# Performance work log

Measured on AMD Instinct MI355X. Metric: run time of the kernel, lower is better.

Reference implementation:

```python
import jax, jax.numpy as jnp
import numpy as np

B, T, C = 4, 2048, 1024
H, D = 16, 64  # num_heads, head_dim; H*D == C

def setup_inputs() -> dict:
    key = jax.random.key(0)
    ks = jax.random.split(key, 5)
    s = 0.02
    return {
        "x": jax.random.normal(ks[0], (B, T, C), dtype=jnp.float32),
        "W_qkv": jax.random.normal(ks[1], (C, 3 * C), dtype=jnp.float32) * s,
        "b_qkv": jnp.zeros((3 * C,), dtype=jnp.float32),
        "W_out": jax.random.normal(ks[2], (C, C), dtype=jnp.float32) * s,
        "b_out": jnp.zeros((C,), dtype=jnp.float32),
    }

def reference(x, W_qkv, b_qkv, W_out, b_out):
    Bx, Tx, Cx = x.shape
    qkv = x @ W_qkv + b_qkv                       # [B,T,3C]
    q, k, v = jnp.split(qkv, 3, axis=-1)
    def heads(t):
        return t.reshape(Bx, Tx, H, D).transpose(0, 2, 1, 3)  # [B,H,T,D]
    q, k, v = heads(q), heads(k), heads(v)
    scale = 1.0 / jnp.sqrt(jnp.float32(D))
    attn = jnp.einsum('bhqd,bhkd->bhqk', q, k) * scale
    causal = jnp.tril(jnp.ones((Tx, Tx), dtype=bool))  # True = keep
    attn = jnp.where(causal, attn, -jnp.inf)
    attn = jax.nn.softmax(attn, axis=-1)
    out = jnp.einsum('bhqk,bhkd->bhqd', attn, v)  # [B,H,T,D]
    out = out.transpose(0, 2, 1, 3).reshape(Bx, Tx, Cx)
    return out @ W_out + b_out
```

## Files before the change

### kernel.cpp

```cpp
#include <hip/hip_runtime.h>
#include <math.h>

typedef unsigned short u16;
using bf16x8   = __attribute__((ext_vector_type(8))) __bf16;
using floatx4  = __attribute__((ext_vector_type(4))) float;
using ushortx8 = __attribute__((ext_vector_type(8))) unsigned short;
using ushortx4 = __attribute__((ext_vector_type(4))) unsigned short;
using uintx4   = __attribute__((ext_vector_type(4))) unsigned int;
using uintx2   = __attribute__((ext_vector_type(2))) unsigned int;

static __device__ __forceinline__ u16 f2bf(float f) {
  return (u16)((__float_as_uint(f) + 0x8000u) >> 16);
}
static __device__ __forceinline__ unsigned int pk2bf(float lo, float hi) {
#if __has_builtin(__builtin_amdgcn_cvt_pk_bf16_f32)
  typedef __attribute__((ext_vector_type(2))) __bf16 bf16x2_t;
  bf16x2_t r = __builtin_amdgcn_cvt_pk_bf16_f32(lo, hi);
  return *(unsigned int*)&r;
#else
  return __builtin_amdgcn_perm(__float_as_uint(hi) + 0x8000u,
                               __float_as_uint(lo) + 0x8000u, 0x07060302u);
#endif
}
static __device__ __forceinline__ float fast_exp2(float x) {
#if __has_builtin(__builtin_amdgcn_exp2f)
  return __builtin_amdgcn_exp2f(x);
#else
  return exp2f(x);
#endif
}
static __device__ __forceinline__ float fast_rcp(float x) {
#if __has_builtin(__builtin_amdgcn_rcpf)
  return __builtin_amdgcn_rcpf(x);
#else
  return 1.0f / x;
#endif
}
static __device__ __forceinline__ void gload_lds16(const void* g, void* l) {
  __builtin_amdgcn_global_load_lds(
      (const __attribute__((address_space(1))) unsigned int*)g,
      (__attribute__((address_space(3))) unsigned int*)l, 16, 0, 0);
}

static __device__ __forceinline__ void transW_tile(
    const float* __restrict__ W, u16* __restrict__ WT, int K, int N,
    int bx, int by, float (*tile)[68], int t) {
  const int kb = by * 64, nb = bx * 64;
  {
    const int kl = t >> 2, nc = (t & 3) * 16;
    const float* src = W + (size_t)(kb + kl) * N + nb + nc;
    #pragma unroll
    for (int c = 0; c < 4; c++)
      *(floatx4*)&tile[kl][nc + c * 4] = *(const floatx4*)(src + c * 4);
  }
  __syncthreads();
  {
    const int nl = t >> 2, kc = (t & 3) * 16;
    uintx4 u0, u1;
    #pragma unroll
    for (int j = 0; j < 4; j++)
      u0[j] = pk2bf(tile[kc + 2 * j][nl], tile[kc + 2 * j + 1][nl]);
    #pragma unroll
    for (int j = 0; j < 4; j++)
      u1[j] = pk2bf(tile[kc + 8 + 2 * j][nl], tile[kc + 9 + 2 * j][nl]);
    u16* dst = WT + (size_t)(nb + nl) * K + kb + kc;
    *(uintx4*)dst = u0;
    *(uintx4*)(dst + 8) = u1;
  }
}

__global__ __launch_bounds__(256) void prep(
    const float* __restrict__ x, const float* __restrict__ Wqkv,
    const float* __restrict__ Wout, u16* __restrict__ Xb,
    u16* __restrict__ WqT, u16* __restrict__ WoT) {
  __shared__ float tile[64][68];
  const int blk = blockIdx.x;
  const int t = threadIdx.x;
  if (blk < 4096) {
    const int i = (blk * 256 + t) * 8;
    floatx4 f0 = *(const floatx4*)(x + i);
    floatx4 f1 = *(const floatx4*)(x + i + 4);
    uintx4 u;
    u[0] = pk2bf(f0[0], f0[1]); u[1] = pk2bf(f0[2], f0[3]);
    u[2] = pk2bf(f1[0], f1[1]); u[3] = pk2bf(f1[2], f1[3]);
    *(uintx4*)(Xb + i) = u;
  } else if (blk < 4096 + 768) {
    const int b2 = blk - 4096;
    transW_tile(Wqkv, WqT, 1024, 3072, b2 % 48, b2 / 48, tile, t);
  } else {
    const int b3 = blk - 4096 - 768;
    transW_tile(Wout, WoT, 1024, 1024, b3 % 16, b3 / 16, tile, t);
  }
}

template <int OUT>
__global__ __launch_bounds__(256) void gemm128(
    const u16* __restrict__ A, const u16* __restrict__ Bt,
    const float* __restrict__ bias,
    u16* __restrict__ Qb, u16* __restrict__ Kb, u16* __restrict__ Vt,
    float* __restrict__ Out, int N, int K)
{
  __shared__ u16 As[128 * 64];
  __shared__ u16 Bs[128 * 64];

  const int tid  = threadIdx.x;
  const int wave = tid >> 6, lane = tid & 63;
  const int quad = lane >> 4, l15 = lane & 15;
  const int lrow = lane >> 3;
  const int scol = ((lane & 7) ^ lrow) * 8;

  const int rowBase = blockIdx.y * 128;
  const int colBase = blockIdx.x * 128;
  const int wRow = (wave >> 1) * 64;
  const int wCol = (wave & 1) * 64;

  floatx4 acc[4][4];
  #pragma unroll
  for (int i = 0; i < 4; i++)
    #pragma unroll
    for (int j = 0; j < 4; j++)
      acc[i][j] = floatx4{0.f, 0.f, 0.f, 0.f};

  const u16* Ap = A  + (size_t)(rowBase + (wave * 4) * 8 + lrow) * K + scol;
  const u16* Bp = Bt + (size_t)(colBase + (wave * 4) * 8 + lrow) * K + scol;

  const bool swapped = (OUT == 1) || (colBase < 2048);

  if (swapped) {
    for (int k0 = 0; k0 < K; k0 += 64) {
      __syncthreads();
      #pragma unroll
      for (int i = 0; i < 4; i++) {
        const int c = wave * 4 + i;
        gload_lds16(Ap + (size_t)(i * 8) * K + k0, &As[c * 512]);
        gload_lds16(Bp + (size_t)(i * 8) * K + k0, &Bs[c * 512]);
      }
      __syncthreads();
      #pragma unroll
      for (int ks = 0; ks < 2; ks++) {
        const int sw = (((ks << 2) | quad) ^ (l15 & 7)) << 3;
        bf16x8 a[4], b[4];
        #pragma unroll
        for (int mt = 0; mt < 4; mt++)
          a[mt] = *(const bf16x8*)&As[(wRow + mt * 16 + l15) * 64 + sw];
        #pragma unroll
        for (int nt = 0; nt < 4; nt++)
          b[nt] = *(const bf16x8*)&Bs[(wCol + nt * 16 + l15) * 64 + sw];
        #pragma unroll
        for (int nt = 0; nt < 4; nt++)
          #pragma unroll
          for (int mt = 0; mt < 4; mt++)
            acc[nt][mt] = __builtin_amdgcn_mfma_f32_16x16x32_bf16(b[nt], a[mt], acc[nt][mt], 0, 0, 0);
      }
    }
    if constexpr (OUT == 0) {
      const int which = colBase >> 10;
      const float qscale = 0.18033688011112042f;
      #pragma unroll
      for (int nt = 0; nt < 4; nt++) {
        const int gn0 = colBase + wCol + nt * 16 + quad * 4;
        const floatx4 bv = *(const floatx4*)&bias[gn0];
        const int gl0 = (gn0 & 1023);
        const int h = gl0 >> 6, d0 = gl0 & 63;
        #pragma unroll
        for (int mt = 0; mt < 4; mt++) {
          const int gm = rowBase + wRow + mt * 16 + l15;
          const int bb = gm >> 11, t0 = gm & 2047;
          const int bh = bb * 16 + h;
          uintx2 w;
          if (which == 0) {
            w[0] = pk2bf((acc[nt][mt][0] + bv[0]) * qscale, (acc[nt][mt][1] + bv[1]) * qscale);
            w[1] = pk2bf((acc[nt][mt][2] + bv[2]) * qscale, (acc[nt][mt][3] + bv[3]) * qscale);
            *(uintx2*)&Qb[((size_t)bh * 2048 + t0) * 64 + d0] = w;
          } else {
            w[0] = pk2bf(acc[nt][mt][0] + bv[0], acc[nt][mt][1] + bv[1]);
            w[1] = pk2bf(acc[nt][mt][2] + bv[2], acc[nt][mt][3] + bv[3]);
            *(uintx2*)&Kb[((size_t)bh * 2048 + t0) * 64 + d0] = w;
          }
        }
      }
    } else {
      #pragma unroll
      for (int nt = 0; nt < 4; nt++) {
        const int gn0 = colBase + wCol + nt * 16 + quad * 4;
        const floatx4 bv = *(const floatx4*)&bias[gn0];
        #pragma unroll
        for (int mt = 0; mt < 4; mt++) {
          const int gm = rowBase + wRow + mt * 16 + l15;
          floatx4 v = acc[nt][mt] + bv;
          *(floatx4*)&Out[(size_t)gm * N + gn0] = v;
        }
      }
    }
  } else {
    for (int k0 = 0; k0 < K; k0 += 64) {
      __syncthreads();
      #pragma unroll
      for (int i = 0; i < 4; i++) {
        const int c = wave * 4 + i;
        gload_lds16(Ap + (size_t)(i * 8) * K + k0, &As[c * 512]);
        gload_lds16(Bp + (size_t)(i * 8) * K + k0, &Bs[c * 512]);
      }
      __syncthreads();
      #pragma unroll
      for (int ks = 0; ks < 2; ks++) {
        const int sw = (((ks << 2) | quad) ^ (l15 & 7)) << 3;
        bf16x8 a[4], b[4];
        #pragma unroll
        for (int mt = 0; mt < 4; mt++)
          a[mt] = *(const bf16x8*)&As[(wRow + mt * 16 + l15) * 64 + sw];
        #pragma unroll
        for (int nt = 0; nt < 4; nt++)
          b[nt] = *(const bf16x8*)&Bs[(wCol + nt * 16 + l15) * 64 + sw];
        #pragma unroll
        for (int mt = 0; mt < 4; mt++)
          #pragma unroll
          for (int nt = 0; nt < 4; nt++)
            acc[mt][nt] = __builtin_amdgcn_mfma_f32_16x16x32_bf16(a[mt], b[nt], acc[mt][nt], 0, 0, 0);
      }
    }
    #pragma unroll
    for (int mt = 0; mt < 4; mt++) {
      const int gm0 = rowBase + wRow + mt * 16 + quad * 4;
      const int bb = gm0 >> 11, t0 = gm0 & 2047;
      #pragma unroll
      for (int nt = 0; nt < 4; nt++) {
        const int gn = colBase + wCol + nt * 16 + l15;
        const int gl = gn & 1023;
        const float bv = bias[gn];
        const int h = gl >> 6, d = gl & 63;
        const int bh = bb * 16 + h;
        uintx2 w;
        w[0] = pk2bf(acc[mt][nt][0] + bv, acc[mt][nt][1] + bv);
        w[1] = pk2bf(acc[mt][nt][2] + bv, acc[mt][nt][3] + bv);
        *(uintx2*)&Vt[((size_t)bh * 64 + d) * 2048 + t0] = w;
      }
    }
  }
}

__global__ __launch_bounds__(256) void attn_fa(
    const u16* __restrict__ Qb, const u16* __restrict__ Kb,
    const u16* __restrict__ Vt, u16* __restrict__ Ob)
{
  __shared__ u16 Qs[128 * 64];
  __shared__ u16 Ks[2][64 * 64], Vs[2][64 * 64];

  const int tid  = threadIdx.x;
  const int wave = tid >> 6, lane = tid & 63;
  const int quad = lane >> 4, l15 = lane & 15;
  const int lrow = lane >> 3;
  const int scol = ((lane & 7) ^ lrow) * 8;

  u16* Pt = &Qs[wave * 16 * 72];

  const int bh    = blockIdx.x;
  const int qt    = 15 - (int)blockIdx.y;
  const int qbase = qt * 128;

  const u16* Qp = Qb + (size_t)bh * 2048 * 64;
  const u16* Kp = Kb + (size_t)bh * 2048 * 64;
  const u16* Vp = Vt + (size_t)bh * 64 * 2048;

  #pragma unroll
  for (int i = 0; i < 4; i++) {
    const int c = wave * 4 + i;
    gload_lds16(Qp + (size_t)(qbase + c * 8 + lrow) * 64 + scol, &Qs[c * 512]);
  }
  #pragma unroll
  for (int i = 0; i < 2; i++) {
    const int c = wave * 2 + i;
    gload_lds16(Kp + (size_t)(c * 8 + lrow) * 64 + scol, &Ks[0][c * 512]);
    gload_lds16(Vp + (size_t)(c * 8 + lrow) * 2048 + scol, &Vs[0][c * 512]);
  }
  __syncthreads();

  const int swA0 = (quad ^ (l15 & 7)) * 8;
  const int swA1 = ((4 + quad) ^ (l15 & 7)) * 8;
  bf16x8 aq[2][2];
  #pragma unroll
  for (int mt = 0; mt < 2; mt++) {
    const int row = wave * 32 + mt * 16 + l15;
    aq[mt][0] = *(const bf16x8*)&Qs[row * 64 + swA0];
    aq[mt][1] = *(const bf16x8*)&Qs[row * 64 + swA1];
  }
  __syncthreads();

  floatx4 o[2][4];
  #pragma unroll
  for (int mt = 0; mt < 2; mt++)
    #pragma unroll
    for (int dt = 0; dt < 4; dt++) o[mt][dt] = floatx4{0.f, 0.f, 0.f, 0.f};
  float lsum[2] = {0.f, 0.f};

  const int rowmax = qbase + wave * 32 + 31;
  const int nk = 2 * qt + 2;
  for (int kt = 0; kt < nk; kt++) {
    const int kbase = kt * 64;
    const int cur = kt & 1;
    if (kt + 1 < nk) {
      const int nb = kbase + 64;
      #pragma unroll
      for (int i = 0; i < 2; i++) {
        const int c = wave * 2 + i;
        gload_lds16(Kp + (size_t)(nb + c * 8 + lrow) * 64 + scol, &Ks[cur ^ 1][c * 512]);
        gload_lds16(Vp + (size_t)(c * 8 + lrow) * 2048 + nb + scol, &Vs[cur ^ 1][c * 512]);
      }
    }

    if (kbase <= rowmax) {
      bf16x8 kf[4][2], vf[4][2];
      #pragma unroll
      for (int ct = 0; ct < 4; ct++) {
        const int row = ct * 16 + l15;
        kf[ct][0] = *(const bf16x8*)&Ks[cur][row * 64 + swA0];
        kf[ct][1] = *(const bf16x8*)&Ks[cur][row * 64 + swA1];
        vf[ct][0] = *(const bf16x8*)&Vs[cur][row * 64 + swA0];
        vf[ct][1] = *(const bf16x8*)&Vs[cur][row * 64 + swA1];
      }

      #pragma unroll
      for (int mt = 0; mt < 2; mt++) {
        const int rowmin = qbase + wave * 32 + mt * 16;
        if (kbase <= rowmin + 15) {
          const bool needmask = (kbase + 63 > rowmin);

          floatx4 st[4];
          #pragma unroll
          for (int ct = 0; ct < 4; ct++) {
            floatx4 z = floatx4{0.f, 0.f, 0.f, 0.f};
            z      = __builtin_amdgcn_mfma_f32_16x16x32_bf16(kf[ct][0], aq[mt][0], z, 0, 0, 0);
            st[ct] = __builtin_amdgcn_mfma_f32_16x16x32_bf16(kf[ct][1], aq[mt][1], z, 0, 0, 0);
          }

          const int qg = rowmin + l15;
          float ls = 0.f;
          #pragma unroll
          for (int ct = 0; ct < 4; ct++) {
            float p0 = fast_exp2(st[ct][0]), p1 = fast_exp2(st[ct][1]);
            float p2 = fast_exp2(st[ct][2]), p3 = fast_exp2(st[ct][3]);
            if (needmask) {
              const int k0i = kbase + ct * 16 + quad * 4;
              if (k0i + 0 > qg) p0 = 0.f;
              if (k0i + 1 > qg) p1 = 0.f;
              if (k0i + 2 > qg) p2 = 0.f;
              if (k0i + 3 > qg) p3 = 0.f;
            }
            ls += (p0 + p1) + (p2 + p3);
            uintx2 w;
            w[0] = pk2bf(p0, p1);
            w[1] = pk2bf(p2, p3);
            *(uintx2*)&Pt[l15 * 72 + ct * 16 + quad * 4] = w;
          }
          lsum[mt] += ls;

          const bf16x8 pb0 = *(const bf16x8*)&Pt[l15 * 72 + quad * 8];
          const bf16x8 pb1 = *(const bf16x8*)&Pt[l15 * 72 + 32 + quad * 8];
          #pragma unroll
          for (int dt = 0; dt < 4; dt++) {
            o[mt][dt] = __builtin_amdgcn_mfma_f32_16x16x32_bf16(vf[dt][0], pb0, o[mt][dt], 0, 0, 0);
            o[mt][dt] = __builtin_amdgcn_mfma_f32_16x16x32_bf16(vf[dt][1], pb1, o[mt][dt], 0, 0, 0);
          }
        }
      }
    }
    __syncthreads();
  }

  const int bb = bh >> 4, h = bh & 15;
  #pragma unroll
  for (int mt = 0; mt < 2; mt++) {
    float l = lsum[mt];
    l += __shfl_xor(l, 16);
    l += __shfl_xor(l, 32);
    const float linv = fast_rcp(l);
    const int t = qbase + wave * 32 + mt * 16 + l15;
    u16* dst = Ob + ((size_t)(bb * 2048 + t)) * 1024 + h * 64 + quad * 4;
    #pragma unroll
    for (int dt = 0; dt < 4; dt++) {
      uintx2 w;
      w[0] = pk2bf(o[mt][dt][0] * linv, o[mt][dt][1] * linv);
      w[1] = pk2bf(o[mt][dt][2] * linv, o[mt][dt][3] * linv);
      *(uintx2*)(dst + dt * 16) = w;
    }
  }
}

extern "C" void kernel_launch(void* const* d_in, const int* in_sizes, int n_in,
                              void* d_out, int out_size, void* d_ws, size_t ws_size,
                              hipStream_t stream) {
  const float* x    = (const float*)d_in[0];
  const float* Wqkv = (const float*)d_in[1];
  const float* bqkv = (const float*)d_in[2];
  const float* Wout = (const float*)d_in[3];
  const float* bout = (const float*)d_in[4];

  const size_t NB = (size_t)8192 * 1024;
  u16* Xb  = (u16*)d_ws;
  u16* WqT = Xb + NB;
  u16* WoT = WqT + (size_t)3072 * 1024;
  u16* Qb  = WoT + (size_t)1024 * 1024;
  u16* Kb  = Qb + NB;
  u16* Vt  = Kb + NB;

  prep<<<5120, 256, 0, stream>>>(x, Wqkv, Wout, Xb, WqT, WoT);
  gemm128<0><<<dim3(24, 64), 256, 0, stream>>>(
      Xb, WqT, bqkv, Qb, Kb, Vt, nullptr, 3072, 1024);
  attn_fa<<<dim3(64, 16), 256, 0, stream>>>(Qb, Kb, Vt, Xb);
  gemm128<1><<<dim3(8, 64), 256, 0, stream>>>(
      Xb, WoT, bout, nullptr, nullptr, nullptr, (float*)d_out, 1024, 1024);
}
```

Before: 255.3 us.

## Batch QK MFMAs across row tiles and swizzle P scratch; unify QKV GEMM path

In the attention kernel, both row tiles' QK^T MFMAs are issued together before the softmax and PV phases. Per-row-tile skip checks are dropped, and P is written to a separate XOR-swizzled LDS buffer per row tile, which is meant to improve MFMA/ALU interleaving and reduce LDS bank conflicts. The QKV projection GEMM now always uses the non-swapped MFMA orientation, with scalar or 4-wide bf16 epilogue stores for Q, K and V. This trades coalesced packed Q/K stores for scattered 2-byte writes, and fully masked row tiles now do redundant work.

```diff
diff --git a/kernel.cpp b/kernel.cpp
--- a/kernel.cpp
+++ b/kernel.cpp
@@ -124,28 +124,33 @@
   const u16* Ap = A  + (size_t)(rowBase + (wave * 4) * 8 + lrow) * K + scol;
   const u16* Bp = Bt + (size_t)(colBase + (wave * 4) * 8 + lrow) * K + scol;
 
-  const bool swapped = (OUT == 1) || (colBase < 2048);
-
-  if (swapped) {
-    for (int k0 = 0; k0 < K; k0 += 64) {
-      __syncthreads();
-      #pragma unroll
-      for (int i = 0; i < 4; i++) {
-        const int c = wave * 4 + i;
-        gload_lds16(Ap + (size_t)(i * 8) * K + k0, &As[c * 512]);
-        gload_lds16(Bp + (size_t)(i * 8) * K + k0, &Bs[c * 512]);
-      }
-      __syncthreads();
-      #pragma unroll
-      for (int ks = 0; ks < 2; ks++) {
-        const int sw = (((ks << 2) | quad) ^ (l15 & 7)) << 3;
-        bf16x8 a[4], b[4];
+  for (int k0 = 0; k0 < K; k0 += 64) {
+    __syncthreads();
+    #pragma unroll
+    for (int i = 0; i < 4; i++) {
+      const int c = wave * 4 + i;
+      gload_lds16(Ap + (size_t)(i * 8) * K + k0, &As[c * 512]);
+      gload_lds16(Bp + (size_t)(i * 8) * K + k0, &Bs[c * 512]);
+    }
+    __syncthreads();
+
+    #pragma unroll
+    for (int ks = 0; ks < 2; ks++) {
+      const int sw = (((ks << 2) | quad) ^ (l15 & 7)) << 3;
+      bf16x8 a[4], b[4];
+      #pragma unroll
+      for (int mt = 0; mt < 4; mt++)
+        a[mt] = *(const bf16x8*)&As[(wRow + mt * 16 + l15) * 64 + sw];
+      #pragma unroll
+      for (int nt = 0; nt < 4; nt++)
+        b[nt] = *(const bf16x8*)&Bs[(wCol + nt * 16 + l15) * 64 + sw];
+      if constexpr (OUT == 0) {
         #pragma unroll
         for (int mt = 0; mt < 4; mt++)
-          a[mt] = *(const bf16x8*)&As[(wRow + mt * 16 + l15) * 64 + sw];
-        #pragma unroll
-        for (int nt = 0; nt < 4; nt++)
-          b[nt] = *(const bf16x8*)&Bs[(wCol + nt * 16 + l15) * 64 + sw];
+          #pragma unroll
+          for (int nt = 0; nt < 4; nt++)
+            acc[mt][nt] = __builtin_amdgcn_mfma_f32_16x16x32_bf16(a[mt], b[nt], acc[mt][nt], 0, 0, 0);
+      } else {
         #pragma unroll
         for (int nt = 0; nt < 4; nt++)
           #pragma unroll
@@ -153,72 +158,12 @@
             acc[nt][mt] = __builtin_amdgcn_mfma_f32_16x16x32_bf16(b[nt], a[mt], acc[nt][mt], 0, 0, 0);
       }
     }
-    if constexpr (OUT == 0) {
-      const int which = colBase >> 10;
-      const float qscale = 0.18033688011112042f;
-      #pragma unroll
-      for (int nt = 0; nt < 4; nt++) {
-        const int gn0 = colBase + wCol + nt * 16 + quad * 4;
-        const floatx4 bv = *(const floatx4*)&bias[gn0];
-        const int gl0 = (gn0 & 1023);
-        const int h = gl0 >> 6, d0 = gl0 & 63;
-        #pragma unroll
-        for (int mt = 0; mt < 4; mt++) {
-          const int gm = rowBase + wRow + mt * 16 + l15;
-          const int bb = gm >> 11, t0 = gm & 2047;
-          const int bh = bb * 16 + h;
-          uintx2 w;
-          if (which == 0) {
-            w[0] = pk2bf((acc[nt][mt][0] + bv[0]) * qscale, (acc[nt][mt][1] + bv[1]) * qscale);
-            w[1] = pk2bf((acc[nt][mt][2] + bv[2]) * qscale, (acc[nt][mt][3] + bv[3]) * qscale);
-            *(uintx2*)&Qb[((size_t)bh * 2048 + t0) * 64 + d0] = w;
-          } else {
-            w[0] = pk2bf(acc[nt][mt][0] + bv[0], acc[nt][mt][1] + bv[1]);
-            w[1] = pk2bf(acc[nt][mt][2] + bv[2], acc[nt][mt][3] + bv[3]);
-            *(uintx2*)&Kb[((size_t)bh * 2048 + t0) * 64 + d0] = w;
-          }
-        }
-      }
-    } else {
-      #pragma unroll
-      for (int nt = 0; nt < 4; nt++) {
-        const int gn0 = colBase + wCol + nt * 16 + quad * 4;
-        const floatx4 bv = *(const floatx4*)&bias[gn0];
-        #pragma unroll
-        for (int mt = 0; mt < 4; mt++) {
-          const int gm = rowBase + wRow + mt * 16 + l15;
-          floatx4 v = acc[nt][mt] + bv;
-          *(floatx4*)&Out[(size_t)gm * N + gn0] = v;
-        }
-      }
-    }
-  } else {
-    for (int k0 = 0; k0 < K; k0 += 64) {
-      __syncthreads();
-      #pragma unroll
-      for (int i = 0; i < 4; i++) {
-        const int c = wave * 4 + i;
-        gload_lds16(Ap + (size_t)(i * 8) * K + k0, &As[c * 512]);
-        gload_lds16(Bp + (size_t)(i * 8) * K + k0, &Bs[c * 512]);
-      }
-      __syncthreads();
-      #pragma unroll
-      for (int ks = 0; ks < 2; ks++) {
-        const int sw = (((ks << 2) | quad) ^ (l15 & 7)) << 3;
-        bf16x8 a[4], b[4];
-        #pragma unroll
-        for (int mt = 0; mt < 4; mt++)
-          a[mt] = *(const bf16x8*)&As[(wRow + mt * 16 + l15) * 64 + sw];
-        #pragma unroll
-        for (int nt = 0; nt < 4; nt++)
-          b[nt] = *(const bf16x8*)&Bs[(wCol + nt * 16 + l15) * 64 + sw];
-        #pragma unroll
-        for (int mt = 0; mt < 4; mt++)
-          #pragma unroll
-          for (int nt = 0; nt < 4; nt++)
-            acc[mt][nt] = __builtin_amdgcn_mfma_f32_16x16x32_bf16(a[mt], b[nt], acc[mt][nt], 0, 0, 0);
-      }
-    }
+  }
+
+  if constexpr (OUT == 0) {
+    const int which = colBase >> 10;
+    const int cb = colBase & 1023;
+    const float qscale = 0.18033688011112042f;
     #pragma unroll
     for (int mt = 0; mt < 4; mt++) {
       const int gm0 = rowBase + wRow + mt * 16 + quad * 4;
@@ -226,14 +171,36 @@
       #pragma unroll
       for (int nt = 0; nt < 4; nt++) {
         const int gn = colBase + wCol + nt * 16 + l15;
-        const int gl = gn & 1023;
+        const int gl = cb + wCol + nt * 16 + l15;
         const float bv = bias[gn];
         const int h = gl >> 6, d = gl & 63;
         const int bh = bb * 16 + h;
-        uintx2 w;
-        w[0] = pk2bf(acc[mt][nt][0] + bv, acc[mt][nt][1] + bv);
-        w[1] = pk2bf(acc[mt][nt][2] + bv, acc[mt][nt][3] + bv);
-        *(uintx2*)&Vt[((size_t)bh * 64 + d) * 2048 + t0] = w;
+        if (which == 2) {
+          ushortx4 pk;
+          #pragma unroll
+          for (int r = 0; r < 4; r++) pk[r] = f2bf(acc[mt][nt][r] + bv);
+          *(ushortx4*)&Vt[((size_t)bh * 64 + d) * 2048 + t0] = pk;
+        } else if (which == 0) {
+          #pragma unroll
+          for (int r = 0; r < 4; r++)
+            Qb[((size_t)bh * 2048 + t0 + r) * 64 + d] = f2bf((acc[mt][nt][r] + bv) * qscale);
+        } else {
+          #pragma unroll
+          for (int r = 0; r < 4; r++)
+            Kb[((size_t)bh * 2048 + t0 + r) * 64 + d] = f2bf(acc[mt][nt][r] + bv);
+        }
+      }
+    }
+  } else {
+    #pragma unroll
+    for (int nt = 0; nt < 4; nt++) {
+      const int gn0 = colBase + wCol + nt * 16 + quad * 4;
+      const floatx4 bv = *(const floatx4*)&bias[gn0];
+      #pragma unroll
+      for (int mt = 0; mt < 4; mt++) {
+        const int gm = rowBase + wRow + mt * 16 + l15;
+        floatx4 v = acc[nt][mt] + bv;
+        *(floatx4*)&Out[(size_t)gm * N + gn0] = v;
       }
     }
   }
@@ -252,8 +219,6 @@
   const int lrow = lane >> 3;
   const int scol = ((lane & 7) ^ lrow) * 8;
 
-  u16* Pt = &Qs[wave * 16 * 72];
-
   const int bh    = blockIdx.x;
   const int qt    = 15 - (int)blockIdx.y;
   const int qbase = qt * 128;
@@ -285,6 +250,11 @@
     aq[mt][1] = *(const bf16x8*)&Qs[row * 64 + swA1];
   }
   __syncthreads();
+
+  u16* Pt0 = &Qs[(wave * 2 + 0) * 1024];
+  u16* Pt1 = &Qs[(wave * 2 + 1) * 1024];
+  const int pwr = l15 * 64 + (quad & 1) * 4;
+  const int pw_x = (quad >> 1);
 
   floatx4 o[2][4];
   #pragma unroll
@@ -309,12 +279,28 @@
     }
 
     if (kbase <= rowmax) {
-      bf16x8 kf[4][2], vf[4][2];
+      bf16x8 kf[4][2];
       #pragma unroll
       for (int ct = 0; ct < 4; ct++) {
         const int row = ct * 16 + l15;
         kf[ct][0] = *(const bf16x8*)&Ks[cur][row * 64 + swA0];
         kf[ct][1] = *(const bf16x8*)&Ks[cur][row * 64 + swA1];
+      }
+
+      floatx4 st[2][4];
+      #pragma unroll
+      for (int mt = 0; mt < 2; mt++)
+        #pragma unroll
+        for (int ct = 0; ct < 4; ct++) {
+          floatx4 z = floatx4{0.f, 0.f, 0.f, 0.f};
+          z          = __builtin_amdgcn_mfma_f32_16x16x32_bf16(kf[ct][0], aq[mt][0], z, 0, 0, 0);
+          st[mt][ct] = __builtin_amdgcn_mfma_f32_16x16x32_bf16(kf[ct][1], aq[mt][1], z, 0, 0, 0);
+        }
+
+      bf16x8 vf[4][2];
+      #pragma unroll
+      for (int ct = 0; ct < 4; ct++) {
+        const int row = ct * 16 + l15;
         vf[ct][0] = *(const bf16x8*)&Vs[cur][row * 64 + swA0];
         vf[ct][1] = *(const bf16x8*)&Vs[cur][row * 64 + swA1];
       }
@@ -322,45 +308,40 @@
       #pragma unroll
       for (int mt = 0; mt < 2; mt++) {
         const int rowmin = qbase + wave * 32 + mt * 16;
-        if (kbase <= rowmin + 15) {
-          const bool needmask = (kbase + 63 > rowmin);
-
-          floatx4 st[4];
-          #pragma unroll
-          for (int ct = 0; ct < 4; ct++) {
-            floatx4 z = floatx4{0.f, 0.f, 0.f, 0.f};
-            z      = __builtin_amdgcn_mfma_f32_16x16x32_bf16(kf[ct][0], aq[mt][0], z, 0, 0, 0);
-            st[ct] = __builtin_amdgcn_mfma_f32_16x16x32_bf16(kf[ct][1], aq[mt][1], z, 0, 0, 0);
+        const bool needmask = (kbase + 63 > rowmin);
+        const int qg = rowmin + l15;
+        u16* Ptm = mt ? Pt1 : Pt0;
+        float ls = 0.f;
+        #pragma unroll
+        for (int ct = 0; ct < 4; ct++) {
+          float p0 = fast_exp2(st[mt][ct][0]), p1 = fast_exp2(st[mt][ct][1]);
+          float p2 = fast_exp2(st[mt][ct][2]), p3 = fast_exp2(st[mt][ct][3]);
+          if (needmask) {
+            const int k0i = kbase + ct * 16 + quad * 4;
+            if (k0i + 0 > qg) p0 = 0.f;
+            if (k0i + 1 > qg) p1 = 0.f;
+            if (k0i + 2 > qg) p2 = 0.f;
+            if (k0i + 3 > qg) p3 = 0.f;
           }
-
-          const int qg = rowmin + l15;
-          float ls = 0.f;
-          #pragma unroll
-          for (int ct = 0; ct < 4; ct++) {
-            float p0 = fast_exp2(st[ct][0]), p1 = fast_exp2(st[ct][1]);
-            float p2 = fast_exp2(st[ct][2]), p3 = fast_exp2(st[ct][3]);
-            if (needmask) {
-              const int k0i = kbase + ct * 16 + quad * 4;
-              if (k0i + 0 > qg) p0 = 0.f;
-              if (k0i + 1 > qg) p1 = 0.f;
-              if (k0i + 2 > qg) p2 = 0.f;
-              if (k0i + 3 > qg) p3 = 0.f;
-            }
-            ls += (p0 + p1) + (p2 + p3);
-            uintx2 w;
-            w[0] = pk2bf(p0, p1);
-            w[1] = pk2bf(p2, p3);
-            *(uintx2*)&Pt[l15 * 72 + ct * 16 + quad * 4] = w;
-          }
-          lsum[mt] += ls;
-
-          const bf16x8 pb0 = *(const bf16x8*)&Pt[l15 * 72 + quad * 8];
-          const bf16x8 pb1 = *(const bf16x8*)&Pt[l15 * 72 + 32 + quad * 8];
-          #pragma unroll
-          for (int dt = 0; dt < 4; dt++) {
-            o[mt][dt] = __builtin_amdgcn_mfma_f32_16x16x32_bf16(vf[dt][0], pb0, o[mt][dt], 0, 0, 0);
-            o[mt][dt] = __builtin_amdgcn_mfma_f32_16x16x32_bf16(vf[dt][1], pb1, o[mt][dt], 0, 0, 0);
-          }
+          ls += (p0 + p1) + (p2 + p3);
+          uintx2 w;
+          w[0] = pk2bf(p0, p1);
+          w[1] = pk2bf(p2, p3);
+          const int chunk = ct * 2 + pw_x;
+          *(uintx2*)&Ptm[pwr + ((chunk ^ (l15 & 7)) << 3)] = w;
+        }
+        lsum[mt] += ls;
+      }
+
+      #pragma unroll
+      for (int mt = 0; mt < 2; mt++) {
+        u16* Ptm = mt ? Pt1 : Pt0;
+        const bf16x8 pb0 = *(const bf16x8*)&Ptm[l15 * 64 + swA0];
+        const bf16x8 pb1 = *(const bf16x8*)&Ptm[l15 * 64 + swA1];
+        #pragma unroll
+        for (int dt = 0; dt < 4; dt++) {
+          o[mt][dt] = __builtin_amdgcn_mfma_f32_16x16x32_bf16(vf[dt][0], pb0, o[mt][dt], 0, 0, 0);
+          o[mt][dt] = __builtin_amdgcn_mfma_f32_16x16x32_bf16(vf[dt][1], pb1, o[mt][dt], 0, 0, 0);
         }
       }
     }
```

New measurement: 256.9 us. No clear change (+0.6%).
